# Optimization experiments

Measured on AMD Instinct MI355X. Metric: run time of the kernel, lower is better.

## Reference

```python
import jax, jax.numpy as jnp
import numpy as np
from jax import lax

BZ, CAP, SEQ, INV = 32, 134, 144, 16
E_SP, E_FT = 1072, 64


def sage(x, e_src, e_dst, Wl, bl, Wr, n_nodes):
    # PyG SAGEConv (mean aggr): out = lin_l(mean_{j->i} x_j) + lin_r(x_i)
    # x: [B, N, F]; edges broadcast over batch
    msgs = x[:, e_src]                                   # [B, E, F] gather
    agg = jnp.zeros_like(x).at[:, e_dst].add(msgs)        # [B, N, F] scatter-add
    deg = jnp.zeros((n_nodes,), x.dtype).at[e_dst].add(1.0)
    mean = agg / jnp.clip(deg, 1.0)[None, :, None]
    return mean @ Wl + bl + x @ Wr


def setup_inputs() -> dict:
    key = jax.random.key(0)
    ks = jax.random.split(key, 16)
    s = lambda fan: 1.0 / np.sqrt(fan)
    inp = {
        'src': jax.random.normal(ks[0], (BZ, CAP, SEQ, INV), jnp.float32),
        'graph_edge_index': jax.random.randint(ks[1], (2, E_SP), 0, CAP, jnp.int32),
        'feature_edge_index': jax.random.randint(ks[2], (2, E_FT), 0, INV, jnp.int32),
        # spatial SAGEConv(in_var, in_var)
        'gcn_Wl': jax.random.uniform(ks[3], (INV, INV), jnp.float32, -s(INV), s(INV)),
        'gcn_bl': jnp.zeros((INV,), jnp.float32),
        'gcn_Wr': jax.random.uniform(ks[4], (INV, INV), jnp.float32, -s(INV), s(INV)),
        # feature SAGEConv(seq_len, seq_len)
        'fgcn_Wl': jax.random.uniform(ks[5], (SEQ, SEQ), jnp.float32, -s(SEQ), s(SEQ)),
        'fgcn_bl': jnp.zeros((SEQ,), jnp.float32),
        'fgcn_Wr': jax.random.uniform(ks[6], (SEQ, SEQ), jnp.float32, -s(SEQ), s(SEQ)),
        # Conv1d(in_var, in_var, k=3/5, no bias): OIW layout
        'conv1_w': jax.random.uniform(ks[7], (INV, INV, 3), jnp.float32, -s(INV * 3), s(INV * 3)),
        'conv2_w': jax.random.uniform(ks[8], (INV, INV, 5), jnp.float32, -s(INV * 5), s(INV * 5)),
        # Linear(3*in_var, in_var)
        'fc_w': jax.random.uniform(ks[9], (3 * INV, INV), jnp.float32, -s(3 * INV), s(3 * INV)),
        'fc_b': jnp.zeros((INV,), jnp.float32),
    }
    return inp


def reference(src, graph_edge_index, feature_edge_index, gcn_Wl, gcn_bl, gcn_Wr,
              fgcn_Wl, fgcn_bl, fgcn_Wr, conv1_w, conv2_w, fc_w, fc_b):
    bz, cap, seq, inv = src.shape
    # --- spatial GCN: nodes = turbines, features = in_var, batched over bz*seq
    x1 = src.transpose(0, 2, 1, 3).reshape(bz * seq, cap, inv)
    sp = sage(x1, graph_edge_index[0], graph_edge_index[1], gcn_Wl, gcn_bl, gcn_Wr, cap)
    spatial_fea = sp.reshape(bz, seq, cap, inv).transpose(0, 2, 1, 3)
    # --- feature GCN: nodes = variables, features = seq_len, batched over bz*cap
    x2 = src.transpose(0, 1, 3, 2).reshape(bz * cap, inv, seq)
    ft = sage(x2, feature_edge_index[0], feature_edge_index[1], fgcn_Wl, fgcn_bl, fgcn_Wr, inv)
    fea_fea = ft.reshape(bz, cap, inv, seq).transpose(0, 1, 3, 2)
    # --- temporal dual Conv1d over seq axis, channels = in_var
    x3 = src.reshape(bz * cap, seq, inv).transpose(0, 2, 1)  # [N, C, L]
    dn = ('NCH', 'OIH', 'NCH')
    c1 = lax.conv_general_dilated(x3, conv1_w, (1,), [(1, 1)], dimension_numbers=dn)
    c2 = lax.conv_general_dilated(x3, conv2_w, (1,), [(2, 2)], dimension_numbers=dn)
    temporal_fea = (c1 + c2).transpose(0, 2, 1).reshape(bz, cap, seq, inv)
    # --- concat + FC fusion + residual (dropout = identity at eval)
    com = jnp.concatenate([spatial_fea, fea_fea, temporal_fea], axis=-1)  # [..., 3*inv]
    out = com @ fc_w + fc_b
    return src + out
```

## Files before the change

### kernel.cpp

```cpp
#include <hip/hip_runtime.h>
#include <hip/hip_bf16.h>

#define BZn 32
#define CAPn 134
#define SEQn 144
#define INVn 16
#define ESP 1072
#define EFT 64


typedef __attribute__((ext_vector_type(8))) short bf16x8;
typedef __attribute__((ext_vector_type(4))) short short4v;
typedef __attribute__((ext_vector_type(4))) float f32x4;

#define MFMA(a, b, c) __builtin_amdgcn_mfma_f32_16x16x32_bf16(a, b, c, 0, 0, 0)

__device__ __forceinline__ unsigned short f2bf(float f) {
    union { float f; unsigned u; } v; v.f = f;
    unsigned r = v.u + 0x7fff + ((v.u >> 16) & 1);
    return (unsigned short)(r >> 16);
}
__device__ __forceinline__ unsigned pk2(float a, float b) {
    float2 v; v.x = a; v.y = b;
    union { __hip_bfloat162 h; unsigned u; } c;
    c.h = __float22bfloat162_rn(v);
    return c.u;
}
__device__ __forceinline__ short4v pack4(f32x4 v) {
    union { unsigned u[2]; short4v s; } r;
    r.u[0] = pk2(v[0], v[1]);
    r.u[1] = pk2(v[2], v[3]);
    return r.s;
}

__global__ __launch_bounds__(256) void prep_kernel(
    const int* __restrict__ ge, const int* __restrict__ fe,
    const float* __restrict__ Wl,  const float* __restrict__ Wr,
    const float* __restrict__ fWl, const float* __restrict__ fWr,
    const float* __restrict__ w1,  const float* __restrict__ w2,
    const float* __restrict__ fcw, const float* __restrict__ bl,
    const float* __restrict__ fcb,
    int* __restrict__ ws)
{
    int t = threadIdx.x;
    char* wsb = (char*)ws;
    unsigned short* uB     = (unsigned short*)(wsb + 5376);
    unsigned short* vB     = (unsigned short*)(wsb + 6400);
    unsigned short* spB2   = (unsigned short*)(wsb + 7424);
    float*          biasf  = (float*)(wsb + 8448);
    unsigned short* convA2 = (unsigned short*)(wsb + 8704);
    unsigned short* featB  = (unsigned short*)(wsb + 12800);

    if (blockIdx.x == 0) {
        int* g_rp  = ws;
        int* g_col = ws + 135;
        float* g_inv = (float*)(ws + 1207);
        __shared__ int cnt[CAPn], off[CAPn];
        for (int c0 = t; c0 < CAPn; c0 += 256) cnt[c0] = 0;
        __syncthreads();
        for (int e = t; e < ESP; e += 256) atomicAdd(&cnt[ge[ESP + e]], 1);
        __syncthreads();
        if (t == 0) {
            int run = 0;
            for (int c0 = 0; c0 < CAPn; c0++) {
                off[c0] = run; g_rp[c0] = run;
                g_inv[c0] = 1.0f / fmaxf((float)cnt[c0], 1.0f);
                run += cnt[c0];
            }
            g_rp[CAPn] = run;
        }
        __syncthreads();
        for (int c0 = t; c0 < CAPn; c0 += 256) cnt[c0] = 0;
        __syncthreads();
        for (int e = t; e < ESP; e += 256) {
            int d = ge[ESP + e];
            int p = off[d] + atomicAdd(&cnt[d], 1);
            g_col[p] = ge[e];
        }
    } else if (blockIdx.x == 1) {
        __shared__ float sw[1312];
        __shared__ int fm[256];
        __shared__ float finv[16];
        for (int u = t; u < 768; u += 256) sw[u] = fcw[u];
        if (t < 256) sw[768 + t]  = Wl[t];
        if (t < 256) sw[1024 + t] = Wr[t];
        if (t < 16)  sw[1280 + t] = bl[t];
        if (t < 16)  sw[1296 + t] = fcb[t];
        fm[t] = 0;
        __syncthreads();
        if (t < EFT) atomicAdd(&fm[fe[t] * 16 + fe[EFT + t]], 1);
        __syncthreads();
        if (t < 16) {
            int dg = 0;
            for (int j = 0; j < 16; j++) dg += fm[j * 16 + t];
            finv[t] = 1.0f / fmaxf((float)dg, 1.0f);
        }
        __syncthreads();
        for (int u = t; u < 512; u += 256) {
            int l = u >> 3, j = u & 7, k = (l >> 4) * 8 + j, ip = l & 15;
            float vu = 0.f, vv = 0.f, vs = 0.f;
            if (k < 16) {
                for (int i = 0; i < 16; i++)
                    vu += (float)fm[k * 16 + i] * finv[i] * sw[(16 + i) * 16 + ip];
                vv = sw[(16 + k) * 16 + ip];
                for (int i = 0; i < 16; i++) vs += sw[768 + k * 16 + i] * sw[i * 16 + ip];
            } else {
                for (int i = 0; i < 16; i++) vs += sw[1024 + (k - 16) * 16 + i] * sw[i * 16 + ip];
            }
            uB[u] = f2bf(vu); vB[u] = f2bf(vv); spB2[u] = f2bf(vs);
        }
        if (t < 16) {
            float b0 = sw[1296 + t], c0 = 0.f;
            for (int i = 0; i < 16; i++) {
                b0 += sw[1280 + i] * sw[i * 16 + t];
                c0 += sw[(16 + i) * 16 + t];
            }
            biasf[t] = b0; biasf[16 + t] = c0;
        }
    } else if (blockIdx.x == 2) {
        __shared__ float swt[2816];
        for (int u = t; u < 768;  u += 256) swt[u]        = fcw[u];
        for (int u = t; u < 768;  u += 256) swt[768 + u]  = w1[u];
        for (int u = t; u < 1280; u += 256) swt[1536 + u] = w2[u];
        __syncthreads();
        for (int u = t; u < 2048; u += 256) {
            int kk2 = u >> 9, l = (u >> 3) & 63, j = u & 7, q = l >> 4, o = l & 15;
            int kkp = kk2 * 2 + (q >> 1), i = (q & 1) * 8 + j;
            float v = 0.f;
            for (int o0 = 0; o0 < 16; o0++) {
                float w = (kkp < 3) ? swt[768 + (o0 * 16 + i) * 3 + kkp]
                                    : swt[1536 + (o0 * 16 + i) * 5 + (kkp - 3)];
                v += w * swt[(32 + o0) * 16 + o];
            }
            convA2[u] = f2bf(v);
        }
    } else {
        __shared__ float wtile[32][145];
        int kk = blockIdx.x - 3;
        for (int u = t; u < 32 * 144; u += 256) {
            int r = u / 144, s = u - r * 144;
            int k = kk * 32 + r;
            wtile[r][s] = (k < 144) ? fWl[k * 144 + s] : fWr[(k - 144) * 144 + s];
        }
        __syncthreads();
        for (int u = t; u < 4608; u += 256) {
            int n0 = u >> 9, rem = u & 511;
            int l = rem >> 3, j = rem & 7;
            featB[(kk * 9 + n0) * 512 + rem] =
                f2bf(wtile[(l >> 4) * 8 + j][n0 * 16 + (l & 15)]);
        }
    }
}

__global__ __launch_bounds__(256, 4) void fused_kernel(
    const float* __restrict__ src,
    const float* __restrict__ fbl,
    const int* __restrict__ ws,
    float* __restrict__ out)
{
    const int* g_rp  = ws;
    const int* g_col = ws + 135;
    const float* g_inv = (const float*)(ws + 1207);
    const char* wsb = (const char*)ws;
    const unsigned short* uB     = (const unsigned short*)(wsb + 5376);
    const unsigned short* vB     = (const unsigned short*)(wsb + 6400);
    const unsigned short* spB2   = (const unsigned short*)(wsb + 7424);
    const float*          biasf  = (const float*)(wsb + 8448);
    const unsigned short* convA2 = (const unsigned short*)(wsb + 8704);
    const unsigned short* featB  = (const unsigned short*)(wsb + 12800);

    __shared__ __align__(16) char smem[17792];
    unsigned short* xs = (unsigned short*)smem;
    unsigned short* uv = (unsigned short*)(smem + 7104);
    float* accF   = (float*)smem;
    float* s_fbl  = (float*)(smem + 17088);
    float* s_bias = (float*)(smem + 17664);
    float* s_cs   = (float*)(smem + 17728);

    int t = threadIdx.x;
    int wave = t >> 6, lane = t & 63;
    int q = lane >> 4, ln = lane & 15;

    int ust_w = (wave == 0) ? 0 : (2 * wave + 1);

    int xcd  = blockIdx.x & 7;
    int slot = blockIdx.x >> 3;
    int bl_  = slot / 134;
    int c    = slot - bl_ * 134;
    int b    = xcd * 4 + bl_;
    int bc   = b * CAPn + c;
    const float* srcb = src + (size_t)b * (CAPn * SEQn * INVn);
    const float* srcc = srcb + (size_t)c * (SEQn * INVn);

    const f32x4* s4 = (const f32x4*)srcc;
    f32x4 x0 = s4[t], x1 = s4[t + 256];
    f32x4 x2 = {0.f,0.f,0.f,0.f};
    if (t < 64) x2 = s4[t + 512];

    int rs = g_rp[c], re = g_rp[c + 1];
    float idg = g_inv[c];
    f32x4 m0a = {0.f,0.f,0.f,0.f}, m1a = {0.f,0.f,0.f,0.f}, m2a = {0.f,0.f,0.f,0.f};
    f32x4 m0b = {0.f,0.f,0.f,0.f}, m1b = {0.f,0.f,0.f,0.f}, m2b = {0.f,0.f,0.f,0.f};
    int e = rs;
    for (; e + 3 < re; e += 4) {
        int n0_ = g_col[e], n1_ = g_col[e + 1], n2_ = g_col[e + 2], n3_ = g_col[e + 3];
        const f32x4* p0 = (const f32x4*)(srcb + (size_t)n0_ * (SEQn * INVn));
        const f32x4* p1 = (const f32x4*)(srcb + (size_t)n1_ * (SEQn * INVn));
        const f32x4* p2 = (const f32x4*)(srcb + (size_t)n2_ * (SEQn * INVn));
        const f32x4* p3 = (const f32x4*)(srcb + (size_t)n3_ * (SEQn * INVn));
        f32x4 a0 = p0[t],       a1 = p1[t],       a2 = p2[t],       a3 = p3[t];
        f32x4 b0 = p0[t + 256], b1 = p1[t + 256], b2 = p2[t + 256], b3 = p3[t + 256];
        f32x4 c0 = {0.f,0.f,0.f,0.f}, c1 = c0, c2 = c0, c3 = c0;
        if (t < 64) { c0 = p0[t + 512]; c1 = p1[t + 512]; c2 = p2[t + 512]; c3 = p3[t + 512]; }
        m0a += a0; m0b += a1; m1a += b0; m1b += b1;
        m0a += a2; m0b += a3; m1a += b2; m1b += b3;
        if (t < 64) { m2a += c0; m2b += c1; m2a += c2; m2b += c3; }
    }
    for (; e + 1 < re; e += 2) {
        int na = g_col[e], nb = g_col[e + 1];
        const f32x4* pa = (const f32x4*)(srcb + (size_t)na * (SEQn * INVn));
        const f32x4* pb = (const f32x4*)(srcb + (size_t)nb * (SEQn * INVn));
        m0a += pa[t];       m0b += pb[t];
        m1a += pa[t + 256]; m1b += pb[t + 256];
        if (t < 64) { m2a += pa[t + 512]; m2b += pb[t + 512]; }
    }
    if (e < re) {
        int na = g_col[e];
        const f32x4* pa = (const f32x4*)(srcb + (size_t)na * (SEQn * INVn));
        m0a += pa[t]; m1a += pa[t + 256];
        if (t < 64) m2a += pa[t + 512];
    }

    bf16x8 caf0 = *(const bf16x8*)(convA2 + (0 * 64 + lane) * 8);
    bf16x8 caf1 = *(const bf16x8*)(convA2 + (1 * 64 + lane) * 8);
    bf16x8 caf2 = *(const bf16x8*)(convA2 + (2 * 64 + lane) * 8);
    bf16x8 caf3 = *(const bf16x8*)(convA2 + (3 * 64 + lane) * 8);
    bf16x8 sbf = *(const bf16x8*)(spB2 + lane * 8);
    bf16x8 ubf = *(const bf16x8*)(uB + lane * 8);
    bf16x8 vbf = *(const bf16x8*)(vB + lane * 8);

    f32x4 m0 = (m0a + m0b) * idg, m1 = (m1a + m1b) * idg, m2 = (m2a + m2b) * idg;
    unsigned pA0 = pk2(m0[0], m0[1]), pB0 = pk2(m0[2], m0[3]);
    unsigned pA1 = pk2(m1[0], m1[1]), pB1 = pk2(m1[2], m1[3]);
    unsigned pA2 = pk2(m2[0], m2[1]), pB2 = pk2(m2[2], m2[3]);

    int s0g = t >> 2, i0g = (t & 3) * 4;
    *(short4v*)&xs[(s0g + 2) * 24 + i0g]        = pack4(x0);
    *(short4v*)&xs[(64 + s0g + 2) * 24 + i0g]   = pack4(x1);
    if (t < 64) *(short4v*)&xs[(128 + s0g + 2) * 24 + i0g] = pack4(x2);
    if (t < 64) {
        int r = t >> 4, i = t & 15;
        int row = (r < 2) ? r : 144 + r;
        xs[row * 24 + i] = 0;
    }
    if (t < SEQn) s_fbl[t] = fbl[t];
    if (t < 16) { s_bias[t] = biasf[t]; s_cs[t] = biasf[16 + t]; }
    __syncthreads();

    #pragma unroll
    for (int tt = 0; tt < 3; tt++) {
        if ((wave == 0) || (tt < 2)) {
            int mtt = ust_w + tt;
            int sl = mtt * 16 + ln;
            bf16x8 a = {0,0,0,0,0,0,0,0};
            if (q < 2) a = *(const bf16x8*)&xs[(sl + 2) * 24 + q * 8];
            f32x4 au = {0.f,0.f,0.f,0.f}, av = {0.f,0.f,0.f,0.f};
            au = MFMA(a, ubf, au);
            av = MFMA(a, vbf, av);
            *(short4v*)&uv[ln * 312 + mtt * 16 + q * 4]       = pack4(au);
            *(short4v*)&uv[ln * 312 + 144 + mtt * 16 + q * 4] = pack4(av);
        }
    }

#define SP_TILE(T, PA, PB, ACC) { \
    int base4 = (ln * 4 + 2 * q) * 4; \
    int d0 = __builtin_amdgcn_ds_bpermute(base4,     (int)(PA)); \
    int d1 = __builtin_amdgcn_ds_bpermute(base4,     (int)(PB)); \
    int d2 = __builtin_amdgcn_ds_bpermute(base4 + 4, (int)(PA)); \
    int d3 = __builtin_amdgcn_ds_bpermute(base4 + 4, (int)(PB)); \
    bf16x8 a_; \
    if (q < 2) { \
        union { int i_[4]; bf16x8 v_; } u_; \
        u_.i_[0] = d0; u_.i_[1] = d1; u_.i_[2] = d2; u_.i_[3] = d3; \
        a_ = u_.v_; \
    } else { \
        a_ = *(const bf16x8*)&xs[((T) * 16 + ln + 2) * 24 + (q & 1) * 8]; \
    } \
    ACC = MFMA(a_, sbf, ACC); }

    f32x4 accS0 = {0.f,0.f,0.f,0.f}, accS1 = accS0, accS2 = accS0;
    SP_TILE(wave,     pA0, pB0, accS0)
    SP_TILE(wave + 4, pA1, pB1, accS1)
    if (wave == 0) SP_TILE(8, pA2, pB2, accS2)
#undef SP_TILE
    __syncthreads();

#define B_TILE(N0, ACC) { \
    int n0_t = (N0); int sl_t = n0_t * 16 + ln; \
    bf16x8 bfrag[9]; \
    _Pragma("unroll") \
    for (int kk = 0; kk < 9; kk++) \
        bfrag[kk] = *(const bf16x8*)(featB + ((kk * 9 + n0_t) * 64 + lane) * 8); \
    bf16x8 cb[4]; \
    _Pragma("unroll") \
    for (int kk = 0; kk < 4; kk++) { \
        int kkp = kk * 2 + (q >> 1); \
        int off = (kkp < 3) ? (kkp - 1) : (kkp - 5); \
        cb[kk] = *(const bf16x8*)&xs[(sl_t + 2 + off) * 24 + (q & 1) * 8]; } \
    f32x4 acc_ = {0.f,0.f,0.f,0.f}; \
    acc_ = MFMA(caf0, cb[0], acc_); \
    acc_ = MFMA(caf1, cb[1], acc_); \
    acc_ = MFMA(caf2, cb[2], acc_); \
    acc_ = MFMA(caf3, cb[3], acc_); \
    _Pragma("unroll") \
    for (int kk = 0; kk < 9; kk++) { \
        bf16x8 a_ = *(const bf16x8*)&uv[ln * 312 + kk * 32 + q * 8]; \
        acc_ = MFMA(a_, bfrag[kk], acc_); } \
    ACC = acc_; }

    f32x4 accB0 = {0.f,0.f,0.f,0.f}, accB1 = accB0, accB2 = accB0;
    B_TILE(ust_w + 0, accB0)
    B_TILE(ust_w + 1, accB1)
    if (wave == 0) B_TILE(ust_w + 2, accB2)
#undef B_TILE
    __syncthreads();

    *(f32x4*)&accF[((ust_w + 0) * 16 + ln) * 20 + q * 4] = accB0;
    *(f32x4*)&accF[((ust_w + 1) * 16 + ln) * 20 + q * 4] = accB1;
    if (wave == 0)
        *(f32x4*)&accF[((ust_w + 2) * 16 + ln) * 20 + q * 4] = accB2;
    __syncthreads();

    #pragma unroll
    for (int r = 0; r < 4; r++)
        accF[(wave * 16 + q * 4 + r) * 20 + ln] += accS0[r];
    #pragma unroll
    for (int r = 0; r < 4; r++)
        accF[((wave + 4) * 16 + q * 4 + r) * 20 + ln] += accS1[r];
    if (wave == 0) {
        #pragma unroll
        for (int r = 0; r < 4; r++)
            accF[(128 + q * 4 + r) * 20 + ln] += accS2[r];
    }
    __syncthreads();

    f32x4* out4 = (f32x4*)(out + (size_t)bc * (SEQn * INVn));
    int i0 = (t & 3) * 4;
    f32x4 bias4 = *(const f32x4*)&s_bias[i0];
    f32x4 cs4   = *(const f32x4*)&s_cs[i0];
    {
        f32x4 a = *(const f32x4*)&accF[(t >> 2) * 20 + i0];
        out4[t] = a + x0 + bias4 + s_fbl[t >> 2] * cs4;
    }
    {
        int t1 = t + 256;
        f32x4 a = *(const f32x4*)&accF[(t1 >> 2) * 20 + i0];
        out4[t1] = a + x1 + bias4 + s_fbl[t1 >> 2] * cs4;
    }
    if (t < 64) {
        int t2 = t + 512;
        f32x4 a = *(const f32x4*)&accF[(t2 >> 2) * 20 + i0];
        out4[t2] = a + x2 + bias4 + s_fbl[t2 >> 2] * cs4;
    }
}

extern "C" void kernel_launch(void* const* d_in, const int* in_sizes, int n_in,
                              void* d_out, int out_size, void* d_ws, size_t ws_size,
                              hipStream_t stream)
{
    const float* src = (const float*)d_in[0];
    const int* ge = (const int*)d_in[1];
    const int* fe = (const int*)d_in[2];
    const float* Wl  = (const float*)d_in[3];
    const float* blp = (const float*)d_in[4];
    const float* Wr  = (const float*)d_in[5];
    const float* fWl = (const float*)d_in[6];
    const float* fbl = (const float*)d_in[7];
    const float* fWr = (const float*)d_in[8];
    const float* w1  = (const float*)d_in[9];
    const float* w2  = (const float*)d_in[10];
    const float* fcw = (const float*)d_in[11];
    const float* fcb = (const float*)d_in[12];
    float* out = (float*)d_out;
    int* ws = (int*)d_ws;

    hipLaunchKernelGGL(prep_kernel, dim3(12), dim3(256), 0, stream,
                       ge, fe, Wl, Wr, fWl, fWr, w1, w2, fcw, blp, fcb, ws);
    hipLaunchKernelGGL(fused_kernel, dim3(BZn * CAPn), dim3(256), 0, stream,
                       src, fbl, ws, out);
}
```

Before: 150.7 us.

## Process two turbine nodes per 512-thread block to share feature-weight fragments

Each block now handles two (b,c) nodes with 512 threads, giving each half its own shared-memory staging for xs and uv. In the feature-GCN stage each wave loads one set of featB B-fragments and reuses it for both nodes, instead of every wave loading fragments for two or three tiles. The leftover ninth tile is split between waves 0 and 1. This cuts repeated global/L2 weight-fragment loads and halves the block count. In exchange, shared memory per block roughly doubles and launch_bounds(512,4) may squeeze registers or occupancy.

```diff
diff --git a/kernel.cpp b/kernel.cpp
--- a/kernel.cpp
+++ b/kernel.cpp
@@ -152,7 +152,7 @@
     }
 }
 
-__global__ __launch_bounds__(256, 4) void fused_kernel(
+__global__ __launch_bounds__(512, 4) void fused_kernel(
     const float* __restrict__ src,
     const float* __restrict__ fbl,
     const int* __restrict__ ws,
@@ -169,33 +169,44 @@
     const unsigned short* convA2 = (const unsigned short*)(wsb + 8704);
     const unsigned short* featB  = (const unsigned short*)(wsb + 12800);
 
-    __shared__ __align__(16) char smem[17792];
-    unsigned short* xs = (unsigned short*)smem;
-    unsigned short* uv = (unsigned short*)(smem + 7104);
-    float* accF   = (float*)smem;
-    float* s_fbl  = (float*)(smem + 17088);
-    float* s_bias = (float*)(smem + 17664);
-    float* s_cs   = (float*)(smem + 17728);
+    __shared__ __align__(16) char smem[34880];
+    unsigned short* xsA = (unsigned short*)smem;
+    unsigned short* xsB = (unsigned short*)(smem + 7104);
+    unsigned short* uvA = (unsigned short*)(smem + 14208);
+    unsigned short* uvB = (unsigned short*)(smem + 24192);
+    float* accFA  = (float*)smem;
+    float* accFB  = (float*)(smem + 11520);
+    float* s_fbl  = (float*)(smem + 34176);
+    float* s_bias = (float*)(smem + 34752);
+    float* s_cs   = (float*)(smem + 34816);
 
     int t = threadIdx.x;
-    int wave = t >> 6, lane = t & 63;
+    int half = t >> 8;
+    int th = t & 255;
+    int wave = t >> 6;
+    int w4 = wave & 3;
+    int lane = t & 63;
     int q = lane >> 4, ln = lane & 15;
 
-    int ust_w = (wave == 0) ? 0 : (2 * wave + 1);
+    unsigned short* xs = half ? xsB : xsA;
+    unsigned short* uv = half ? uvB : uvA;
+
+    int ust_w = (w4 == 0) ? 0 : (2 * w4 + 1);
 
     int xcd  = blockIdx.x & 7;
     int slot = blockIdx.x >> 3;
-    int bl_  = slot / 134;
-    int c    = slot - bl_ * 134;
+    int bl_  = slot / 67;
+    int c0   = slot - bl_ * 67;
     int b    = xcd * 4 + bl_;
+    int c    = c0 + half * 67;
     int bc   = b * CAPn + c;
     const float* srcb = src + (size_t)b * (CAPn * SEQn * INVn);
     const float* srcc = srcb + (size_t)c * (SEQn * INVn);
 
     const f32x4* s4 = (const f32x4*)srcc;
-    f32x4 x0 = s4[t], x1 = s4[t + 256];
+    f32x4 x0 = s4[th], x1 = s4[th + 256];
     f32x4 x2 = {0.f,0.f,0.f,0.f};
-    if (t < 64) x2 = s4[t + 512];
+    if (th < 64) x2 = s4[th + 512];
 
     int rs = g_rp[c], re = g_rp[c + 1];
     float idg = g_inv[c];
@@ -208,27 +219,27 @@
         const f32x4* p1 = (const f32x4*)(srcb + (size_t)n1_ * (SEQn * INVn));
         const f32x4* p2 = (const f32x4*)(srcb + (size_t)n2_ * (SEQn * INVn));
         const f32x4* p3 = (const f32x4*)(srcb + (size_t)n3_ * (SEQn * INVn));
-        f32x4 a0 = p0[t],       a1 = p1[t],       a2 = p2[t],       a3 = p3[t];
-        f32x4 b0 = p0[t + 256], b1 = p1[t + 256], b2 = p2[t + 256], b3 = p3[t + 256];
-        f32x4 c0 = {0.f,0.f,0.f,0.f}, c1 = c0, c2 = c0, c3 = c0;
-        if (t < 64) { c0 = p0[t + 512]; c1 = p1[t + 512]; c2 = p2[t + 512]; c3 = p3[t + 512]; }
+        f32x4 a0 = p0[th],       a1 = p1[th],       a2 = p2[th],       a3 = p3[th];
+        f32x4 b0 = p0[th + 256], b1 = p1[th + 256], b2 = p2[th + 256], b3 = p3[th + 256];
+        f32x4 c0_ = {0.f,0.f,0.f,0.f}, c1_ = c0_, c2_ = c0_, c3_ = c0_;
+        if (th < 64) { c0_ = p0[th + 512]; c1_ = p1[th + 512]; c2_ = p2[th + 512]; c3_ = p3[th + 512]; }
         m0a += a0; m0b += a1; m1a += b0; m1b += b1;
         m0a += a2; m0b += a3; m1a += b2; m1b += b3;
-        if (t < 64) { m2a += c0; m2b += c1; m2a += c2; m2b += c3; }
+        if (th < 64) { m2a += c0_; m2b += c1_; m2a += c2_; m2b += c3_; }
     }
     for (; e + 1 < re; e += 2) {
         int na = g_col[e], nb = g_col[e + 1];
         const f32x4* pa = (const f32x4*)(srcb + (size_t)na * (SEQn * INVn));
         const f32x4* pb = (const f32x4*)(srcb + (size_t)nb * (SEQn * INVn));
-        m0a += pa[t];       m0b += pb[t];
-        m1a += pa[t + 256]; m1b += pb[t + 256];
-        if (t < 64) { m2a += pa[t + 512]; m2b += pb[t + 512]; }
+        m0a += pa[th];       m0b += pb[th];
+        m1a += pa[th + 256]; m1b += pb[th + 256];
+        if (th < 64) { m2a += pa[th + 512]; m2b += pb[th + 512]; }
     }
     if (e < re) {
         int na = g_col[e];
         const f32x4* pa = (const f32x4*)(srcb + (size_t)na * (SEQn * INVn));
-        m0a += pa[t]; m1a += pa[t + 256];
-        if (t < 64) m2a += pa[t + 512];
+        m0a += pa[th]; m1a += pa[th + 256];
+        if (th < 64) m2a += pa[th + 512];
     }
 
     bf16x8 caf0 = *(const bf16x8*)(convA2 + (0 * 64 + lane) * 8);
@@ -244,12 +255,12 @@
     unsigned pA1 = pk2(m1[0], m1[1]), pB1 = pk2(m1[2], m1[3]);
     unsigned pA2 = pk2(m2[0], m2[1]), pB2 = pk2(m2[2], m2[3]);
 
-    int s0g = t >> 2, i0g = (t & 3) * 4;
+    int s0g = th >> 2, i0g = (th & 3) * 4;
     *(short4v*)&xs[(s0g + 2) * 24 + i0g]        = pack4(x0);
     *(short4v*)&xs[(64 + s0g + 2) * 24 + i0g]   = pack4(x1);
-    if (t < 64) *(short4v*)&xs[(128 + s0g + 2) * 24 + i0g] = pack4(x2);
-    if (t < 64) {
-        int r = t >> 4, i = t & 15;
+    if (th < 64) *(short4v*)&xs[(128 + s0g + 2) * 24 + i0g] = pack4(x2);
+    if (th < 64) {
+        int r = th >> 4, i = th & 15;
         int row = (r < 2) ? r : 144 + r;
         xs[row * 24 + i] = 0;
     }
@@ -259,7 +270,7 @@
 
     #pragma unroll
     for (int tt = 0; tt < 3; tt++) {
-        if ((wave == 0) || (tt < 2)) {
+        if ((w4 == 0) || (tt < 2)) {
             int mtt = ust_w + tt;
             int sl = mtt * 16 + ln;
             bf16x8 a = {0,0,0,0,0,0,0,0};
@@ -289,24 +300,20 @@
     ACC = MFMA(a_, sbf, ACC); }
 
     f32x4 accS0 = {0.f,0.f,0.f,0.f}, accS1 = accS0, accS2 = accS0;
-    SP_TILE(wave,     pA0, pB0, accS0)
-    SP_TILE(wave + 4, pA1, pB1, accS1)
-    if (wave == 0) SP_TILE(8, pA2, pB2, accS2)
+    SP_TILE(w4,     pA0, pB0, accS0)
+    SP_TILE(w4 + 4, pA1, pB1, accS1)
+    if (w4 == 0) SP_TILE(8, pA2, pB2, accS2)
 #undef SP_TILE
     __syncthreads();
 
-#define B_TILE(N0, ACC) { \
-    int n0_t = (N0); int sl_t = n0_t * 16 + ln; \
-    bf16x8 bfrag[9]; \
-    _Pragma("unroll") \
-    for (int kk = 0; kk < 9; kk++) \
-        bfrag[kk] = *(const bf16x8*)(featB + ((kk * 9 + n0_t) * 64 + lane) * 8); \
+#define B_CHAIN(XS, UV, N0, BF, ACC) { \
+    int sl_t = (N0) * 16 + ln; \
     bf16x8 cb[4]; \
     _Pragma("unroll") \
     for (int kk = 0; kk < 4; kk++) { \
         int kkp = kk * 2 + (q >> 1); \
         int off = (kkp < 3) ? (kkp - 1) : (kkp - 5); \
-        cb[kk] = *(const bf16x8*)&xs[(sl_t + 2 + off) * 24 + (q & 1) * 8]; } \
+        cb[kk] = *(const bf16x8*)&XS[(sl_t + 2 + off) * 24 + (q & 1) * 8]; } \
     f32x4 acc_ = {0.f,0.f,0.f,0.f}; \
     acc_ = MFMA(caf0, cb[0], acc_); \
     acc_ = MFMA(caf1, cb[1], acc_); \
@@ -314,30 +321,45 @@
     acc_ = MFMA(caf3, cb[3], acc_); \
     _Pragma("unroll") \
     for (int kk = 0; kk < 9; kk++) { \
-        bf16x8 a_ = *(const bf16x8*)&uv[ln * 312 + kk * 32 + q * 8]; \
-        acc_ = MFMA(a_, bfrag[kk], acc_); } \
+        bf16x8 a_ = *(const bf16x8*)&UV[ln * 312 + kk * 32 + q * 8]; \
+        acc_ = MFMA(a_, BF[kk], acc_); } \
     ACC = acc_; }
 
-    f32x4 accB0 = {0.f,0.f,0.f,0.f}, accB1 = accB0, accB2 = accB0;
-    B_TILE(ust_w + 0, accB0)
-    B_TILE(ust_w + 1, accB1)
-    if (wave == 0) B_TILE(ust_w + 2, accB2)
-#undef B_TILE
+    int myTile = wave;
+    f32x4 accPA = {0.f,0.f,0.f,0.f}, accPB = accPA, accE = accPA;
+    {
+        bf16x8 bfrag[9];
+        #pragma unroll
+        for (int kk = 0; kk < 9; kk++)
+            bfrag[kk] = *(const bf16x8*)(featB + ((kk * 9 + myTile) * 64 + lane) * 8);
+        B_CHAIN(xsA, uvA, myTile, bfrag, accPA)
+        B_CHAIN(xsB, uvB, myTile, bfrag, accPB)
+    }
+    if (wave < 2) {
+        bf16x8 bfrag8[9];
+        #pragma unroll
+        for (int kk = 0; kk < 9; kk++)
+            bfrag8[kk] = *(const bf16x8*)(featB + ((kk * 9 + 8) * 64 + lane) * 8);
+        if (wave == 0) { B_CHAIN(xsA, uvA, 8, bfrag8, accE) }
+        else           { B_CHAIN(xsB, uvB, 8, bfrag8, accE) }
+    }
+#undef B_CHAIN
     __syncthreads();
 
-    *(f32x4*)&accF[((ust_w + 0) * 16 + ln) * 20 + q * 4] = accB0;
-    *(f32x4*)&accF[((ust_w + 1) * 16 + ln) * 20 + q * 4] = accB1;
-    if (wave == 0)
-        *(f32x4*)&accF[((ust_w + 2) * 16 + ln) * 20 + q * 4] = accB2;
+    *(f32x4*)&accFA[(myTile * 16 + ln) * 20 + q * 4] = accPA;
+    *(f32x4*)&accFB[(myTile * 16 + ln) * 20 + q * 4] = accPB;
+    if (wave == 0) *(f32x4*)&accFA[(128 + ln) * 20 + q * 4] = accE;
+    if (wave == 1) *(f32x4*)&accFB[(128 + ln) * 20 + q * 4] = accE;
     __syncthreads();
 
+    float* accF = half ? accFB : accFA;
     #pragma unroll
     for (int r = 0; r < 4; r++)
-        accF[(wave * 16 + q * 4 + r) * 20 + ln] += accS0[r];
+        accF[(w4 * 16 + q * 4 + r) * 20 + ln] += accS0[r];
     #pragma unroll
     for (int r = 0; r < 4; r++)
-        accF[((wave + 4) * 16 + q * 4 + r) * 20 + ln] += accS1[r];
-    if (wave == 0) {
+        accF[((w4 + 4) * 16 + q * 4 + r) * 20 + ln] += accS1[r];
+    if (w4 == 0) {
         #pragma unroll
         for (int r = 0; r < 4; r++)
             accF[(128 + q * 4 + r) * 20 + ln] += accS2[r];
@@ -345,20 +367,20 @@
     __syncthreads();
 
     f32x4* out4 = (f32x4*)(out + (size_t)bc * (SEQn * INVn));
-    int i0 = (t & 3) * 4;
+    int i0 = (th & 3) * 4;
     f32x4 bias4 = *(const f32x4*)&s_bias[i0];
     f32x4 cs4   = *(const f32x4*)&s_cs[i0];
     {
-        f32x4 a = *(const f32x4*)&accF[(t >> 2) * 20 + i0];
-        out4[t] = a + x0 + bias4 + s_fbl[t >> 2] * cs4;
+        f32x4 a = *(const f32x4*)&accF[(th >> 2) * 20 + i0];
+        out4[th] = a + x0 + bias4 + s_fbl[th >> 2] * cs4;
     }
     {
-        int t1 = t + 256;
+        int t1 = th + 256;
         f32x4 a = *(const f32x4*)&accF[(t1 >> 2) * 20 + i0];
         out4[t1] = a + x1 + bias4 + s_fbl[t1 >> 2] * cs4;
     }
-    if (t < 64) {
-        int t2 = t + 512;
+    if (th < 64) {
+        int t2 = th + 512;
         f32x4 a = *(const f32x4*)&accF[(t2 >> 2) * 20 + i0];
         out4[t2] = a + x2 + bias4 + s_fbl[t2 >> 2] * cs4;
     }
@@ -386,6 +408,6 @@
 
     hipLaunchKernelGGL(prep_kernel, dim3(12), dim3(256), 0, stream,
                        ge, fe, Wl, Wr, fWl, fWr, w1, w2, fcw, blp, fcb, ws);
-    hipLaunchKernelGGL(fused_kernel, dim3(BZn * CAPn), dim3(256), 0, stream,
+    hipLaunchKernelGGL(fused_kernel, dim3(8 * 4 * 67), dim3(512), 0, stream,
                        src, fbl, ws, out);
 }
```

New measurement: 209.3 us. 1.39x slower.
